# Optimization experiments

Hardware: AMD Instinct MI355X
Metric: run time of the kernel (lower is better)

## Reference

```python
import jax, jax.numpy as jnp
import numpy as np

B, T, DIN, D = 8, 2048, 512, 1024
LN_EPS = 1e-5


def setup_inputs() -> dict:
    key = jax.random.key(0)
    ks = jax.random.split(key, 4)
    x = jax.random.normal(ks[0], (B, T, DIN), dtype=jnp.float32)
    Wd = jax.random.normal(ks[1], (DIN, D), dtype=jnp.float32) * (1.0 / np.sqrt(DIN))
    bd = jnp.zeros((D,), jnp.float32)  # nn.init.constant_(delta_proj.bias, 0)
    Wb = jax.random.normal(ks[2], (DIN, D), dtype=jnp.float32) * (1.0 / np.sqrt(DIN))
    bb = jax.random.normal(ks[3], (D,), dtype=jnp.float32) * 0.02
    A_log = jnp.log(jnp.linspace(1.0, 16.0, D, dtype=jnp.float32))
    threshold = jnp.ones((D,), jnp.float32)
    gamma = jnp.ones((D,), jnp.float32)
    beta = jnp.zeros((D,), jnp.float32)
    return {"x": x, "Wd": Wd, "bd": bd, "Wb": Wb, "bb": bb,
            "A_log": A_log, "threshold": threshold, "gamma": gamma, "beta": beta}


def reference(x, Wd, bd, Wb, bb, A_log, threshold, gamma, beta):
    # Input-dependent discretization (parallel over B,T)
    delta = jax.nn.softplus(jnp.einsum('btc,cd->btd', x, Wd) + bd)   # [B,T,D]
    b_step = delta * (jnp.einsum('btc,cd->btd', x, Wb) + bb)          # [B,T,D]
    A = jnp.exp(A_log)                                                # [D]
    a_step = jnp.exp(-delta * A)                                      # [B,T,D]

    # Sequential spiking scan with multiplicative threshold reset (fp32)
    def step(h, ab):
        a, b = ab
        h = a * h + b
        s = (h - threshold > 0).astype(h.dtype)  # spike (no grad path)
        h = h * (1.0 - s)                        # reset
        return h, (h, s)

    aT = jnp.swapaxes(a_step, 0, 1)  # [T,B,D]
    bT = jnp.swapaxes(b_step, 0, 1)
    h0 = jnp.zeros((x.shape[0], A.shape[0]), a_step.dtype)
    _, (hT, sT) = jax.lax.scan(step, h0, (aT, bT))
    h_post = jnp.swapaxes(hT, 0, 1)  # [B,T,D]
    spikes = jnp.swapaxes(sT, 0, 1)

    # LayerNorm over last dim (biased variance, as torch)
    mu = jnp.mean(h_post, axis=-1, keepdims=True)
    var = jnp.mean(jnp.square(h_post - mu), axis=-1, keepdims=True)
    out = (h_post - mu) * jax.lax.rsqrt(var + LN_EPS) * gamma + beta
    return out, spikes
```

## Files before the change

kernel.cpp:

```cpp
#include <hip/hip_runtime.h>
#include <math.h>

#define BB   8
#define TT   2048
#define CIN  512
#define DD   1024
#define MM   (BB * TT)

constexpr int BM = 128;
constexpr int BN = 64;
constexpr int BK = 16;

#define NCHUNK 32
#define CLEN   (TT / NCHUNK)
#define WARM   64
#define PF     8
#define NWAVES 8

__device__ __forceinline__ float softplus_f(float z) {
    return fmaxf(z, 0.f) + log1pf(expf(-fabsf(z)));
}

__global__ __launch_bounds__(256) void k1_gemm_act(
    const float* __restrict__ x,
    const float* __restrict__ Wd,
    const float* __restrict__ Wb,
    const float* __restrict__ bd,
    const float* __restrict__ bb,
    const float* __restrict__ A_log,
    float* __restrict__ a_out,
    float* __restrict__ b_out)
{
    __shared__ float xs[BK][BM + 4];
    __shared__ float wds[BK][BN];
    __shared__ float wbs[BK][BN];

    const int tid = threadIdx.x;
    const int n0  = blockIdx.x * BN;
    const int m0  = blockIdx.y * BM;
    const int tx  = tid & 15;
    const int ty  = tid >> 4;

    const int lm = tid >> 1;
    const int lk = (tid & 1) * 8;
    const int wr = tid >> 4;
    const int wc = (tid & 15) * 4;

    float accd[8][4], accb[8][4];
#pragma unroll
    for (int r = 0; r < 8; ++r)
#pragma unroll
        for (int c = 0; c < 4; ++c) { accd[r][c] = 0.f; accb[r][c] = 0.f; }

    const float* xp  = x + (size_t)(m0 + lm) * CIN + lk;
    const float* wdp = Wd + (size_t)wr * DD + n0 + wc;
    const float* wbp = Wb + (size_t)wr * DD + n0 + wc;
    float4 xva = *(const float4*)(xp);
    float4 xvb = *(const float4*)(xp + 4);
    float4 wd0 = *(const float4*)(wdp);
    float4 wb0 = *(const float4*)(wbp);

    for (int k0 = 0; k0 < CIN; k0 += BK) {
        __syncthreads();
        xs[lk + 0][lm] = xva.x;  xs[lk + 1][lm] = xva.y;
        xs[lk + 2][lm] = xva.z;  xs[lk + 3][lm] = xva.w;
        xs[lk + 4][lm] = xvb.x;  xs[lk + 5][lm] = xvb.y;
        xs[lk + 6][lm] = xvb.z;  xs[lk + 7][lm] = xvb.w;
        *(float4*)&wds[wr][wc] = wd0;
        *(float4*)&wbs[wr][wc] = wb0;
        __syncthreads();

        const int kn = k0 + BK;
        if (kn < CIN) {
            xva = *(const float4*)(xp + kn);
            xvb = *(const float4*)(xp + kn + 4);
            wd0 = *(const float4*)(wdp + (size_t)kn * DD);
            wb0 = *(const float4*)(wbp + (size_t)kn * DD);
        }

#pragma unroll
        for (int kk = 0; kk < BK; ++kk) {
            float4 xa  = *(const float4*)&xs[kk][ty * 8];
            float4 xa2 = *(const float4*)&xs[kk][ty * 8 + 4];
            float4 d0  = *(const float4*)&wds[kk][tx * 4];
            float4 c0  = *(const float4*)&wbs[kk][tx * 4];
            float xr[8] = {xa.x, xa.y, xa.z, xa.w, xa2.x, xa2.y, xa2.z, xa2.w};
            float wd[4] = {d0.x, d0.y, d0.z, d0.w};
            float wb[4] = {c0.x, c0.y, c0.z, c0.w};
#pragma unroll
            for (int r = 0; r < 8; ++r) {
                const float xi = xr[r];
#pragma unroll
                for (int c = 0; c < 4; ++c) {
                    accd[r][c] = fmaf(xi, wd[c], accd[r][c]);
                    accb[r][c] = fmaf(xi, wb[c], accb[r][c]);
                }
            }
        }
    }

    const int nc0 = n0 + tx * 4;
    float4 bdq = *(const float4*)(bd + nc0);
    float4 bbq = *(const float4*)(bb + nc0);
    float4 alq = *(const float4*)(A_log + nc0);
    const float* bdv = (const float*)&bdq;
    const float* bbv = (const float*)&bbq;
    float Aq[4] = {expf(alq.x), expf(alq.y), expf(alq.z), expf(alq.w)};

#pragma unroll
    for (int r = 0; r < 8; ++r) {
        const int m = m0 + ty * 8 + r;
        float av[4], bv[4];
#pragma unroll
        for (int j = 0; j < 4; ++j) {
            float zd    = accd[r][j] + bdv[j];
            float delta = softplus_f(zd);
            float zb    = accb[r][j] + bbv[j];
            av[j] = expf(-delta * Aq[j]);
            bv[j] = delta * zb;
        }
        *(float4*)(a_out + (size_t)m * DD + nc0) = make_float4(av[0], av[1], av[2], av[3]);
        *(float4*)(b_out + (size_t)m * DD + nc0) = make_float4(bv[0], bv[1], bv[2], bv[3]);
    }
}


#define WARM_BATCH(AV, BV)                                                \
    {                                                                     \
        _Pragma("unroll")                                                 \
        for (int j = 0; j < PF; ++j) {                                    \
            h.x = fmaf(AV[j].x, h.x, BV[j].x);                            \
            h.y = fmaf(AV[j].y, h.y, BV[j].y);                            \
            h.x = ((h.x - th.x) > 0.f) ? 0.f : h.x;                       \
            h.y = ((h.y - th.y) > 0.f) ? 0.f : h.y;                       \
        }                                                                 \
    }

#define OUT_BATCH(AV, BV)                                                 \
    {                                                                     \
        float2 hj[PF];                                                    \
        _Pragma("unroll")                                                 \
        for (int j = 0; j < PF; ++j) {                                    \
            h.x = fmaf(AV[j].x, h.x, BV[j].x);                            \
            h.y = fmaf(AV[j].y, h.y, BV[j].y);                            \
            const bool kx = (h.x - th.x) > 0.f;                           \
            const bool ky = (h.y - th.y) > 0.f;                           \
            *(float2*)(sp + (size_t)j * DD) =                             \
                make_float2(kx ? 1.f : 0.f, ky ? 1.f : 0.f);              \
            h.x = kx ? 0.f : h.x;                                         \
            h.y = ky ? 0.f : h.y;                                         \
            hj[j] = h;                                                    \
        }                                                                 \
        sp += (size_t)PF * DD;                                            \
        float s[PF], ssq[PF];                                             \
        _Pragma("unroll")                                                 \
        for (int j = 0; j < PF; ++j) {                                    \
            s[j]   = hj[j].x + hj[j].y;                                   \
            ssq[j] = fmaf(hj[j].x, hj[j].x, hj[j].y * hj[j].y);           \
        }                                                                 \
        _Pragma("unroll")                                                 \
        for (int off = 32; off > 0; off >>= 1) {                          \
            _Pragma("unroll")                                             \
            for (int j = 0; j < PF; ++j) {                                \
                s[j]   += __shfl_down(s[j], off);                         \
                ssq[j] += __shfl_down(ssq[j], off);                       \
            }                                                             \
        }                                                                 \
        if (lane == 0) {                                                  \
            _Pragma("unroll")                                             \
            for (int j = 0; j < PF; ++j) {                                \
                psum[wid][j]      = s[j];                                 \
                psum[wid][j + PF] = ssq[j];                               \
            }                                                             \
        }                                                                 \
        __syncthreads();                                                  \
        if (tid < 128) {                                                  \
            const int v = tid >> 3;                                       \
            const int w = tid & 7;                                        \
            float p = psum[w][v];                                         \
            p += __shfl_down(p, 4);                                       \
            p += __shfl_down(p, 2);                                       \
            p += __shfl_down(p, 1);                                       \
            if (w == 0) red[v] = p;                                       \
        }                                                                 \
        __syncthreads();                                                  \
        if (tid < PF) {                                                   \
            const float mu  = red[tid] * (1.0f / DD);                     \
            const float var =                                             \
                fmaxf(red[tid + PF] * (1.0f / DD) - mu * mu, 0.f);        \
            smu[tid]  = mu;                                               \
            sinv[tid] = 1.0f / sqrtf(var + 1e-5f);                        \
        }                                                                 \
        __syncthreads();                                                  \
        _Pragma("unroll")                                                 \
        for (int j = 0; j < PF; ++j) {                                    \
            float2 o;                                                     \
            o.x = (hj[j].x - smu[j]) * sinv[j] * g.x + be.x;              \
            o.y = (hj[j].y - smu[j]) * sinv[j] * g.y + be.y;              \
            *(float2*)(op + (size_t)j * DD) = o;                          \
        }                                                                 \
        op += (size_t)PF * DD;                                            \
    }

__global__ __launch_bounds__(512) void k23_scan_ln(
    const float* __restrict__ a,
    const float* __restrict__ b,
    const float* __restrict__ thr,
    const float* __restrict__ gamma,
    const float* __restrict__ beta,
    float* __restrict__ out,
    float* __restrict__ spikes)
{
    const int tid   = threadIdx.x;
    const int d0    = tid * 2;
    const int chunk = blockIdx.x;
    const int batch = blockIdx.y;
    const int lane  = tid & 63;
    const int wid   = tid >> 6;

    const float2 th = *(const float2*)(thr + d0);
    const float2 g  = *(const float2*)(gamma + d0);
    const float2 be = *(const float2*)(beta + d0);

    const int t0    = chunk * CLEN;
    const int nwarm = (t0 < WARM) ? t0 : WARM;
    const int tw    = t0 - nwarm;
    const int nwb   = nwarm / PF;
    const int ntot  = nwb + CLEN / PF;

    const size_t rowbase = (size_t)batch * TT * DD + d0;
    const float* ap = a + rowbase + (size_t)tw * DD;
    const float* bp = b + rowbase + (size_t)tw * DD;
    float* op = out    + rowbase + (size_t)t0 * DD;
    float* sp = spikes + rowbase + (size_t)t0 * DD;

    __shared__ float psum[NWAVES][17];
    __shared__ float red[2 * PF];
    __shared__ float smu[PF];
    __shared__ float sinv[PF];

    float2 a0[PF], b0[PF], a1[PF], b1[PF];
#pragma unroll
    for (int j = 0; j < PF; ++j) {
        a0[j] = *(const float2*)(ap + (size_t)j * DD);
        b0[j] = *(const float2*)(bp + (size_t)j * DD);
    }
    ap += (size_t)PF * DD; bp += (size_t)PF * DD;

    float2 h = make_float2(0.f, 0.f);
    for (int i = 0; i < ntot; i += 2) {
#pragma unroll
        for (int j = 0; j < PF; ++j) {
            a1[j] = *(const float2*)(ap + (size_t)j * DD);
            b1[j] = *(const float2*)(bp + (size_t)j * DD);
        }
        ap += (size_t)PF * DD; bp += (size_t)PF * DD;

        if (i >= nwb) OUT_BATCH(a0, b0) else WARM_BATCH(a0, b0)

        if (i + 2 < ntot) {
#pragma unroll
            for (int j = 0; j < PF; ++j) {
                a0[j] = *(const float2*)(ap + (size_t)j * DD);
                b0[j] = *(const float2*)(bp + (size_t)j * DD);
            }
            ap += (size_t)PF * DD; bp += (size_t)PF * DD;
        }

        if (i + 1 >= nwb) OUT_BATCH(a1, b1) else WARM_BATCH(a1, b1)
    }
}

extern "C" void kernel_launch(void* const* d_in, const int* in_sizes, int n_in,
                              void* d_out, int out_size, void* d_ws, size_t ws_size,
                              hipStream_t stream) {
    const float* x     = (const float*)d_in[0];
    const float* Wd    = (const float*)d_in[1];
    const float* bd    = (const float*)d_in[2];
    const float* Wb    = (const float*)d_in[3];
    const float* bb    = (const float*)d_in[4];
    const float* A_log = (const float*)d_in[5];
    const float* thr   = (const float*)d_in[6];
    const float* gamma = (const float*)d_in[7];
    const float* beta  = (const float*)d_in[8];

    float* out    = (float*)d_out;
    float* spikes = out + (size_t)MM * DD;
    float* a_ws   = (float*)d_ws;
    float* b_ws   = a_ws + (size_t)MM * DD;

    dim3 g1(DD / BN, MM / BM);
    k1_gemm_act<<<g1, 256, 0, stream>>>(x, Wd, Wb, bd, bb, A_log, a_ws, b_ws);

    dim3 g2(NCHUNK, BB);
    k23_scan_ln<<<g2, 512, 0, stream>>>(a_ws, b_ws, thr, gamma, beta, out, spikes);
}
```

Measured before the change: 633.4 us.

## Replace shuffle-tree LN reduction with LDS transpose and deepen a/b prefetch

The per-row LayerNorm statistics reduction changes. Instead of a 6-step shuffle tree per value followed by a per-wave psum, each thread writes its partial sums into a 512x17 LDS array, and 32-thread groups reduce 16 entries each before finishing with short shuffles. The a/b loads move into each slot so the next batch is fetched while the barrier waits, which keeps two batches in flight. This uses about 34KB of LDS per block, which may lower occupancy. Warm-up batches also always prefetch, which can read past the valid range when ntot is small.

After: 632.4 us. About the same (-0.2%).

```diff
diff --git a/kernel.cpp b/kernel.cpp
--- a/kernel.cpp
+++ b/kernel.cpp
@@ -15,7 +15,6 @@
 #define CLEN   (TT / NCHUNK)
 #define WARM   64
 #define PF     8
-#define NWAVES 8
 
 __device__ __forceinline__ float softplus_f(float z) {
     return fmaxf(z, 0.f) + log1pf(expf(-fabsf(z)));
@@ -125,7 +124,17 @@
 }
 
 
-#define WARM_BATCH(AV, BV)                                                \
+#define PREFETCH(AV, BV)                                                  \
+    {                                                                     \
+        _Pragma("unroll")                                                 \
+        for (int j = 0; j < PF; ++j) {                                    \
+            AV[j] = *(const float2*)(ap + (size_t)j * DD);                \
+            BV[j] = *(const float2*)(bp + (size_t)j * DD);                \
+        }                                                                 \
+        ap += (size_t)PF * DD; bp += (size_t)PF * DD;                     \
+    }
+
+#define WARM_SLOT(AV, BV)                                                 \
     {                                                                     \
         _Pragma("unroll")                                                 \
         for (int j = 0; j < PF; ++j) {                                    \
@@ -136,7 +145,7 @@
         }                                                                 \
     }
 
-#define OUT_BATCH(AV, BV)                                                 \
+#define OUT_SLOT(AV, BV, PFOK)                                            \
     {                                                                     \
         float2 hj[PF];                                                    \
         _Pragma("unroll")                                                 \
@@ -152,36 +161,25 @@
             hj[j] = h;                                                    \
         }                                                                 \
         sp += (size_t)PF * DD;                                            \
-        float s[PF], ssq[PF];                                             \
-        _Pragma("unroll")                                                 \
-        for (int j = 0; j < PF; ++j) {                                    \
-            s[j]   = hj[j].x + hj[j].y;                                   \
-            ssq[j] = fmaf(hj[j].x, hj[j].x, hj[j].y * hj[j].y);           \
-        }                                                                 \
-        _Pragma("unroll")                                                 \
-        for (int off = 32; off > 0; off >>= 1) {                          \
+        _Pragma("unroll")                                                 \
+        for (int j = 0; j < PF; ++j) {                                    \
+            trans[tid][j]      = hj[j].x + hj[j].y;                       \
+            trans[tid][j + PF] = fmaf(hj[j].x, hj[j].x,                   \
+                                      hj[j].y * hj[j].y);                 \
+        }                                                                 \
+        if (PFOK) PREFETCH(AV, BV)                                        \
+        __syncthreads();                                                  \
+        {                                                                 \
+            float p = 0.f;                                                \
             _Pragma("unroll")                                             \
-            for (int j = 0; j < PF; ++j) {                                \
-                s[j]   += __shfl_down(s[j], off);                         \
-                ssq[j] += __shfl_down(ssq[j], off);                       \
-            }                                                             \
-        }                                                                 \
-        if (lane == 0) {                                                  \
-            _Pragma("unroll")                                             \
-            for (int j = 0; j < PF; ++j) {                                \
-                psum[wid][j]      = s[j];                                 \
-                psum[wid][j + PF] = ssq[j];                               \
-            }                                                             \
-        }                                                                 \
-        __syncthreads();                                                  \
-        if (tid < 128) {                                                  \
-            const int v = tid >> 3;                                       \
-            const int w = tid & 7;                                        \
-            float p = psum[w][v];                                         \
+            for (int i2 = 0; i2 < 16; ++i2)                               \
+                p += trans[i2 * 32 + rs][rq];                             \
+            p += __shfl_down(p, 16);                                      \
+            p += __shfl_down(p, 8);                                       \
             p += __shfl_down(p, 4);                                       \
             p += __shfl_down(p, 2);                                       \
             p += __shfl_down(p, 1);                                       \
-            if (w == 0) red[v] = p;                                       \
+            if (rs == 0) red[rq] = p;                                     \
         }                                                                 \
         __syncthreads();                                                  \
         if (tid < PF) {                                                   \
@@ -215,8 +213,8 @@
     const int d0    = tid * 2;
     const int chunk = blockIdx.x;
     const int batch = blockIdx.y;
-    const int lane  = tid & 63;
-    const int wid   = tid >> 6;
+    const int rq    = tid >> 5;
+    const int rs    = tid & 31;
 
     const float2 th = *(const float2*)(thr + d0);
     const float2 g  = *(const float2*)(gamma + d0);
@@ -234,40 +232,22 @@
     float* op = out    + rowbase + (size_t)t0 * DD;
     float* sp = spikes + rowbase + (size_t)t0 * DD;
 
-    __shared__ float psum[NWAVES][17];
+    __shared__ float trans[512][17];
     __shared__ float red[2 * PF];
     __shared__ float smu[PF];
     __shared__ float sinv[PF];
 
     float2 a0[PF], b0[PF], a1[PF], b1[PF];
-#pragma unroll
-    for (int j = 0; j < PF; ++j) {
-        a0[j] = *(const float2*)(ap + (size_t)j * DD);
-        b0[j] = *(const float2*)(bp + (size_t)j * DD);
-    }
-    ap += (size_t)PF * DD; bp += (size_t)PF * DD;
+    PREFETCH(a0, b0)
+    PREFETCH(a1, b1)
 
     float2 h = make_float2(0.f, 0.f);
     for (int i = 0; i < ntot; i += 2) {
-#pragma unroll
-        for (int j = 0; j < PF; ++j) {
-            a1[j] = *(const float2*)(ap + (size_t)j * DD);
-            b1[j] = *(const float2*)(bp + (size_t)j * DD);
-        }
-        ap += (size_t)PF * DD; bp += (size_t)PF * DD;
-
-        if (i >= nwb) OUT_BATCH(a0, b0) else WARM_BATCH(a0, b0)
-
-        if (i + 2 < ntot) {
-#pragma unroll
-            for (int j = 0; j < PF; ++j) {
-                a0[j] = *(const float2*)(ap + (size_t)j * DD);
-                b0[j] = *(const float2*)(bp + (size_t)j * DD);
-            }
-            ap += (size_t)PF * DD; bp += (size_t)PF * DD;
-        }
-
-        if (i + 1 >= nwb) OUT_BATCH(a1, b1) else WARM_BATCH(a1, b1)
+        if (i >= nwb) OUT_SLOT(a0, b0, i + 2 < ntot)
+        else { WARM_SLOT(a0, b0) PREFETCH(a0, b0) }
+
+        if (i + 1 >= nwb) OUT_SLOT(a1, b1, i + 3 < ntot)
+        else { WARM_SLOT(a1, b1) PREFETCH(a1, b1) }
     }
 }
 
```
